# Kernel tuning notes

Measured on AMD Instinct MI355X. Metric: run time of the kernel, lower is better.

The kernel has to match this reference:

```python
import jax, jax.numpy as jnp
import numpy as np

EMBED_DIM = 1024
HEADS = 16
HEAD_DIM = EMBED_DIM // HEADS


def setup_inputs() -> dict:
    key = jax.random.key(0)
    ks = jax.random.split(key, 5)
    B, N, C = 2, 2048, EMBED_DIM
    scale = 1.0 / np.sqrt(C)
    x = jax.random.normal(ks[0], (B, N, C), dtype=jnp.float32)
    W_qkv = jax.random.normal(ks[1], (C, 3 * C), dtype=jnp.float32) * scale
    b_qkv = jax.random.normal(ks[2], (3 * C,), dtype=jnp.float32) * 0.01
    W_out = jax.random.normal(ks[3], (C, C), dtype=jnp.float32) * scale
    b_out = jax.random.normal(ks[4], (C,), dtype=jnp.float32) * 0.01
    return {"x": x, "W_qkv": W_qkv, "b_qkv": b_qkv, "W_out": W_out, "b_out": b_out}


def reference(x, W_qkv, b_qkv, W_out, b_out):
    B, N, C = x.shape
    qkv = x @ W_qkv + b_qkv                      # [B, N, 3C]
    qkv = qkv.reshape(B, N, 3, HEADS, HEAD_DIM)
    qkv = jnp.transpose(qkv, (2, 0, 3, 1, 4))    # [3, B, H, N, d]
    q, k, v = qkv[0], qkv[1], qkv[2]
    attn = jnp.einsum('bhnd,bhmd->bhnm', q, k) / np.sqrt(HEAD_DIM)
    attn = jax.nn.softmax(attn, axis=-1)
    out = jnp.einsum('bhnm,bhmd->bhnd', attn, v)  # [B, H, N, d]
    out = jnp.transpose(out, (0, 2, 1, 3)).reshape(B, N, C)
    return out @ W_out + b_out
```

## Files before the change

### kernel.cpp

```cpp
#include <hip/hip_runtime.h>
#include <stdint.h>

typedef __bf16 bf16_t;
typedef bf16_t bf16x8 __attribute__((ext_vector_type(8)));
typedef bf16_t bf16x2v __attribute__((ext_vector_type(2)));
typedef float f32x4 __attribute__((ext_vector_type(4)));
typedef float f32x16 __attribute__((ext_vector_type(16)));
typedef uint32_t u32x2 __attribute__((ext_vector_type(2)));
typedef uint32_t u32x4 __attribute__((ext_vector_type(4)));

#define BATCH 2
#define SEQ 2048
#define CDIM 1024
#define NH 16
#define HD 64

#define QSCALE 0.18033688011f

__device__ __forceinline__ uint16_t f32_bf16(float f) {
    __bf16 h = (__bf16)f;
    return __builtin_bit_cast(uint16_t, h);
}

__device__ __forceinline__ uint32_t pack_bf16(float a, float b) {
    bf16x2v t;
    t.x = (__bf16)a;
    t.y = (__bf16)b;
    return __builtin_bit_cast(uint32_t, t);
}

__device__ __forceinline__ bf16x8 ld8(const uint16_t* p) {
    return *reinterpret_cast<const bf16x8*>(p);
}

__device__ __forceinline__ void swap32(uint32_t& a, uint32_t& b) {
#if __has_builtin(__builtin_amdgcn_permlane32_swap)
    u32x2 r = __builtin_amdgcn_permlane32_swap(a, b, false, false);
    a = r.x;
    b = r.y;
#else
    asm("v_permlane32_swap_b32 %0, %1" : "+v"(a), "+v"(b));
#endif
}

__device__ __forceinline__ void gld16(const uint16_t* g, uint16_t* l) {
    __builtin_amdgcn_global_load_lds(
        (__attribute__((address_space(1))) void*)(g),
        (__attribute__((address_space(3))) void*)(l), 16, 0, 0);
}

#define LDS_FENCE() asm volatile("s_waitcnt lgkmcnt(0)" ::: "memory")

__global__ __launch_bounds__(256) void prep_kernel(
        const float* __restrict__ x, uint16_t* __restrict__ x_bf,
        const float* __restrict__ Wqkv, uint16_t* __restrict__ wqkvT,
        const float* __restrict__ Wout, uint16_t* __restrict__ woutT) {
    const int bid = blockIdx.x, tid = threadIdx.x;
    if (bid < 4096) {
        int i = (bid * 256 + tid) * 4;
        float4 v = *(const float4*)(x + i);
        ushort4 o;
        o.x = f32_bf16(v.x);
        o.y = f32_bf16(v.y);
        o.z = f32_bf16(v.z);
        o.w = f32_bf16(v.w);
        *(ushort4*)(x_bf + i) = o;
        return;
    }
    __shared__ float tile[32][33];
    const float* in;
    uint16_t* outp;
    int idx, Cc, ncx;
    if (bid < 4096 + 3072) { idx = bid - 4096; in = Wqkv; outp = wqkvT; Cc = 3072; ncx = 96; }
    else                   { idx = bid - 7168; in = Wout; outp = woutT; Cc = 1024; ncx = 32; }
    const int R = 1024;
    int bx = idx % ncx, by = idx / ncx;
    int c0 = bx * 32, r0 = by * 32;
    int tx = tid & 31, ty = tid >> 5;
#pragma unroll
    for (int i = 0; i < 4; i++)
        tile[ty + i * 8][tx] = in[(size_t)(r0 + ty + i * 8) * Cc + c0 + tx];
    __syncthreads();
    const int rr = tid >> 3, seg = tid & 7;
    ushort4 o;
    o.x = f32_bf16(tile[seg * 4 + 0][rr]);
    o.y = f32_bf16(tile[seg * 4 + 1][rr]);
    o.z = f32_bf16(tile[seg * 4 + 2][rr]);
    o.w = f32_bf16(tile[seg * 4 + 3][rr]);
    *(ushort4*)(outp + (size_t)(c0 + rr) * R + r0 + seg * 4) = o;
}

template <int BM, int BN, int MODE>
__global__ __launch_bounds__(256) void gemm_t(
        const uint16_t* __restrict__ A, const uint16_t* __restrict__ Bt, int K,
        const float* __restrict__ bias,
        uint16_t* __restrict__ qw, uint16_t* __restrict__ kw, uint16_t* __restrict__ vt,
        float* __restrict__ out) {
    constexpr int WT_M = BM / 2, WT_N = BN / 2;
    constexpr int MI = WT_M / 16, NJ = WT_N / 16;
    constexpr int ASEG_W = BM / 64, BSEG_W = BN / 64;
    constexpr int AB = 2 * BM * 32 + 2 * BN * 32;
    constexpr int TS = (MODE == 0) ? 4 * 64 * 68 : 0;
    constexpr int SM = AB > TS ? AB : TS;
    __shared__ uint16_t smem[SM];
    uint16_t* As = smem;
    uint16_t* Bs = smem + 2 * BM * 32;

    const int m0 = blockIdx.y * BM, n0 = blockIdx.x * BN;
    const int tid = threadIdx.x;
    const int w = tid >> 6, lane = tid & 63;
    const int quad = lane >> 4, l16 = lane & 15;
    const int wm = (w >> 1) * WT_M, wn = (w & 1) * WT_N;

    const int srow = lane >> 2;
    const int schunk = (lane & 3) ^ (srow & 3);

    const uint16_t* aP[ASEG_W];
    const uint16_t* bP[BSEG_W];
    int aL[ASEG_W], bL[BSEG_W];
#pragma unroll
    for (int s = 0; s < ASEG_W; s++) {
        int seg = w * ASEG_W + s;
        aP[s] = A + (size_t)(m0 + seg * 16 + srow) * K + schunk * 8;
        aL[s] = seg * 512;
    }
#pragma unroll
    for (int s = 0; s < BSEG_W; s++) {
        int seg = w * BSEG_W + s;
        bP[s] = Bt + (size_t)(n0 + seg * 16 + srow) * K + schunk * 8;
        bL[s] = seg * 512;
    }

    auto stage = [&](int buf, int k0) {
#pragma unroll
        for (int s = 0; s < ASEG_W; s++) gld16(aP[s] + k0, As + buf * BM * 32 + aL[s]);
#pragma unroll
        for (int s = 0; s < BSEG_W; s++) gld16(bP[s] + k0, Bs + buf * BN * 32 + bL[s]);
    };

    const int cslot = (quad ^ (l16 & 3)) * 8;
    f32x4 acc[MI][NJ] = {};

    stage(0, 0);
    const int iters = K / 32;
    for (int it = 0; it < iters; ++it) {
        __syncthreads();
        if (it + 1 < iters) stage((it + 1) & 1, (it + 1) * 32);
        const uint16_t* A_ = As + (it & 1) * BM * 32;
        const uint16_t* B_ = Bs + (it & 1) * BN * 32;
        bf16x8 af[MI], bfr[NJ];
#pragma unroll
        for (int i = 0; i < MI; i++) af[i] = ld8(&A_[(wm + i * 16 + l16) * 32 + cslot]);
#pragma unroll
        for (int j = 0; j < NJ; j++) bfr[j] = ld8(&B_[(wn + j * 16 + l16) * 32 + cslot]);
#pragma unroll
        for (int i = 0; i < MI; i++)
#pragma unroll
            for (int j = 0; j < NJ; j++)
                acc[i][j] = __builtin_amdgcn_mfma_f32_16x16x32_bf16(af[i], bfr[j], acc[i][j], 0, 0, 0);
    }

    const int nbase = n0 + wn;
    float bj[NJ];
#pragma unroll
    for (int j = 0; j < NJ; j++) bj[j] = bias[nbase + j * 16 + l16];

    if constexpr (MODE == 1) {
#pragma unroll
        for (int j = 0; j < NJ; j++) {
#pragma unroll
            for (int i = 0; i < MI; i++)
#pragma unroll
                for (int r = 0; r < 4; r++) {
                    int m = m0 + wm + i * 16 + quad * 4 + r;
                    out[(size_t)m * CDIM + nbase + j * 16 + l16] = acc[i][j][r] + bj[j];
                }
        }
    } else {
        __syncthreads();
        uint16_t* T = smem + w * 64 * 68;
        const int gmb = m0 + wm;
        const int b = gmb >> 11, ns0 = gmb & 2047;

        if (nbase < 2048) {
            const int which = nbase >> 10, h = (nbase & 1023) >> 6;
            const float sc = (which == 0) ? QSCALE : 1.0f;
#pragma unroll
            for (int i = 0; i < 4; i++)
#pragma unroll
                for (int j = 0; j < 4; j++)
#pragma unroll
                    for (int r = 0; r < 4; r++)
                        T[(i * 16 + quad * 4 + r) * 68 + j * 16 + l16] =
                            f32_bf16((acc[i][j][r] + bj[j]) * sc);
            LDS_FENCE();
            uint16_t* dst = ((which == 0) ? qw : kw) +
                            (((size_t)b * NH + h) * SEQ + ns0 + lane) * HD;
#pragma unroll
            for (int g = 0; g < 8; g++) {
                bf16x8 v = ld8(&T[lane * 68 + g * 8]);
                *(bf16x8*)(dst + g * 8) = v;
            }
        } else {
#pragma unroll
            for (int i = 0; i < 4; i++)
#pragma unroll
                for (int j = 0; j < 4; j++) {
                    u32x2 pr;
                    pr.x = pack_bf16(acc[i][j][0] + bj[j], acc[i][j][1] + bj[j]);
                    pr.y = pack_bf16(acc[i][j][2] + bj[j], acc[i][j][3] + bj[j]);
                    *(u32x2*)&T[(j * 16 + l16) * 68 + i * 16 + quad * 4] = pr;
                }
            LDS_FENCE();
            const int h = (nbase - 2048) >> 6;
            uint16_t* dst = vt + (((size_t)b * NH + h) * HD + lane) * SEQ + ns0;
#pragma unroll
            for (int g = 0; g < 16; g++) {
                u32x2 d2 = *(const u32x2*)&T[lane * 68 + g * 4];
                *(u32x2*)(dst + g * 4) = d2;
            }
        }
    }
}

__global__ __launch_bounds__(256) void attn_kernel(
        const uint16_t* __restrict__ qg, const uint16_t* __restrict__ kg,
        const uint16_t* __restrict__ vt, uint16_t* __restrict__ og) {
    __shared__ uint16_t Ks[2][128 * 64];
    __shared__ uint16_t Vs[2][64 * 128];

    const int bh = blockIdx.x;
    const int qt = blockIdx.y;
    const int tid = threadIdx.x;
    const int w = tid >> 6, lane = tid & 63;
    const int l32 = lane & 31, hi = lane >> 5;
    const int qrow0 = qt * 128 + w * 32;
    const size_t base = (size_t)bh * SEQ * HD;

    bf16x8 qf[4];
#pragma unroll
    for (int s = 0; s < 4; s++)
        qf[s] = ld8(qg + base + (size_t)(qrow0 + l32) * HD + s * 16 + hi * 8);

    const int krow = lane >> 3;
    const int kch = (lane & 7) ^ krow;
    const int vrow = lane >> 4;
    const uint16_t* ksrc[4];
    const uint16_t* vsrc[4];
#pragma unroll
    for (int s = 0; s < 4; s++) {
        int seg = w * 4 + s;
        ksrc[s] = kg + base + (size_t)(seg * 8 + krow) * HD + kch * 8;
        int vd = seg * 4 + vrow;
        int vch = (lane & 15) ^ (vd & 15);
        vsrc[s] = vt + base + (size_t)vd * SEQ + vch * 8;
    }

    f32x16 o_acc[2] = {};
    f32x16 l_acc = {};
    u32x4 ov;
    ov.x = 0x3F803F80u; ov.y = 0x3F803F80u; ov.z = 0x3F803F80u; ov.w = 0x3F803F80u;
    const bf16x8 ones8 = __builtin_bit_cast(bf16x8, ov);

    auto stage = [&](int buf) {
#pragma unroll
        for (int s = 0; s < 4; s++) {
            int seg = w * 4 + s;
            gld16(ksrc[s], &Ks[buf][seg * 512]);
            ksrc[s] += 128 * HD;
        }
#pragma unroll
        for (int s = 0; s < 4; s++) {
            int seg = w * 4 + s;
            gld16(vsrc[s], &Vs[buf][seg * 512]);
            vsrc[s] += 128;
        }
    };

    stage(0);

    const int kxe = l32 & 7;
    const int vxe = l32 & 15;

    const int NT = SEQ / 128;
    for (int it = 0; it < NT; ++it) {
        __syncthreads();
        if (it + 1 < NT) stage((it + 1) & 1);
        const uint16_t* K_ = Ks[it & 1];
        const uint16_t* V_ = Vs[it & 1];

#pragma unroll
        for (int kvb = 0; kvb < 4; kvb++) {
            f32x16 S = {};
            const uint16_t* Krow = K_ + (kvb * 32 + l32) * 64;
#pragma unroll
            for (int s = 0; s < 4; s++) {
                bf16x8 kf = ld8(Krow + ((2 * s + hi) ^ kxe) * 8);
                S = __builtin_amdgcn_mfma_f32_32x32x16_bf16(kf, qf[s], S, 0, 0, 0);
            }

            uint32_t pk0[4], pk1[4];
#pragma unroll
            for (int c = 0; c < 4; c++) {
                pk0[c] = pack_bf16(__builtin_amdgcn_exp2f(S[4 * c + 0]),
                                   __builtin_amdgcn_exp2f(S[4 * c + 1]));
                pk1[c] = pack_bf16(__builtin_amdgcn_exp2f(S[4 * c + 2]),
                                   __builtin_amdgcn_exp2f(S[4 * c + 3]));
            }

#pragma unroll
            for (int cp = 0; cp < 2; cp++) {
                uint32_t b0 = pk0[2 * cp], b2 = pk0[2 * cp + 1];
                uint32_t b1 = pk1[2 * cp], b3 = pk1[2 * cp + 1];
                swap32(b0, b2);
                swap32(b1, b3);
                u32x4 t;
                t.x = b0; t.y = b1; t.z = b2; t.w = b3;
                bf16x8 pb = __builtin_bit_cast(bf16x8, t);

                l_acc = __builtin_amdgcn_mfma_f32_32x32x16_bf16(ones8, pb, l_acc, 0, 0, 0);
#pragma unroll
                for (int mf = 0; mf < 2; mf++) {
                    int ch = (kvb * 4 + cp * 2 + hi) ^ vxe;
                    bf16x8 vf = ld8(V_ + (mf * 32 + l32) * 128 + ch * 8);
                    o_acc[mf] = __builtin_amdgcn_mfma_f32_32x32x16_bf16(vf, pb, o_acc[mf], 0, 0, 0);
                }
            }
        }
    }

    const int b = bh >> 4, h = bh & 15;
    const float inv = __builtin_amdgcn_rcpf(l_acc[0]);
    const int ns = qrow0 + l32;
    uint16_t* orow = og + (((size_t)b * SEQ + ns) * NH + h) * HD;
#pragma unroll
    for (int mf = 0; mf < 2; mf++)
#pragma unroll
        for (int c = 0; c < 4; c++) {
            u32x2 pr;
            pr.x = pack_bf16(o_acc[mf][4 * c + 0] * inv, o_acc[mf][4 * c + 1] * inv);
            pr.y = pack_bf16(o_acc[mf][4 * c + 2] * inv, o_acc[mf][4 * c + 3] * inv);
            *(u32x2*)(orow + mf * 32 + c * 8 + hi * 4) = pr;
        }
}

extern "C" void kernel_launch(void* const* d_in, const int* in_sizes, int n_in,
                              void* d_out, int out_size, void* d_ws, size_t ws_size,
                              hipStream_t stream) {
    const float* x = (const float*)d_in[0];
    const float* Wqkv = (const float*)d_in[1];
    const float* bqkv = (const float*)d_in[2];
    const float* Wout = (const float*)d_in[3];
    const float* bout = (const float*)d_in[4];
    float* out = (float*)d_out;

    uint16_t* ws = (uint16_t*)d_ws;
    uint16_t* x_bf  = ws;
    uint16_t* wqkvT = x_bf + 4194304;
    uint16_t* woutT = wqkvT + 3145728;
    uint16_t* qw    = woutT + 1048576;
    uint16_t* kw    = qw + 4194304;
    uint16_t* vtw   = kw + 4194304;
    uint16_t* attn  = vtw + 4194304;

    prep_kernel<<<8192, 256, 0, stream>>>(x, x_bf, Wqkv, wqkvT, Wout, woutT);

    gemm_t<128, 128, 0><<<dim3(24, 32), 256, 0, stream>>>(
        x_bf, wqkvT, 1024, bqkv, qw, kw, vtw, nullptr);

    attn_kernel<<<dim3(32, 16), 256, 0, stream>>>(qw, kw, vtw, attn);

    gemm_t<64, 128, 1><<<dim3(8, 64), 256, 0, stream>>>(
        attn, woutT, 1024, bout, nullptr, nullptr, nullptr, out);
}
```

Measured before the change: 185.0 us.

## Software-pipeline QK^T MFMA with softmax and replace ones-MFMA row sum with VALU

```diff
diff --git a/kernel.cpp b/kernel.cpp
--- a/kernel.cpp
+++ b/kernel.cpp
@@ -257,10 +257,7 @@
     }
 
     f32x16 o_acc[2] = {};
-    f32x16 l_acc = {};
-    u32x4 ov;
-    ov.x = 0x3F803F80u; ov.y = 0x3F803F80u; ov.z = 0x3F803F80u; ov.w = 0x3F803F80u;
-    const bf16x8 ones8 = __builtin_bit_cast(bf16x8, ov);
+    float l_red = 0.0f;
 
     auto stage = [&](int buf) {
 #pragma unroll
@@ -281,6 +278,19 @@
 
     const int kxe = l32 & 7;
     const int vxe = l32 & 15;
+    const int krowb = l32 * 64;
+    const int vrowb = l32 * 128;
+    int kco[4];
+#pragma unroll
+    for (int s = 0; s < 4; s++) kco[s] = ((2 * s + hi) ^ kxe) * 8;
+    int vco[4][2];
+#pragma unroll
+    for (int kvb = 0; kvb < 4; kvb++)
+#pragma unroll
+        for (int cp = 0; cp < 2; cp++)
+            vco[kvb][cp] = ((kvb * 4 + cp * 2 + hi) ^ vxe) * 8;
+
+    const f32x16 fzero = {};
 
     const int NT = SEQ / 128;
     for (int it = 0; it < NT; ++it) {
@@ -289,23 +299,53 @@
         const uint16_t* K_ = Ks[it & 1];
         const uint16_t* V_ = Vs[it & 1];
 
+        bf16x8 kf[2][4];
+        f32x16 S[2];
+#pragma unroll
+        for (int s = 0; s < 4; s++) kf[0][s] = ld8(K_ + krowb + kco[s]);
+        S[0] = fzero;
+#pragma unroll
+        for (int s = 0; s < 4; s++)
+            S[0] = __builtin_amdgcn_mfma_f32_32x32x16_bf16(kf[0][s], qf[s], S[0], 0, 0, 0);
+
 #pragma unroll
         for (int kvb = 0; kvb < 4; kvb++) {
-            f32x16 S = {};
-            const uint16_t* Krow = K_ + (kvb * 32 + l32) * 64;
-#pragma unroll
-            for (int s = 0; s < 4; s++) {
-                bf16x8 kf = ld8(Krow + ((2 * s + hi) ^ kxe) * 8);
-                S = __builtin_amdgcn_mfma_f32_32x32x16_bf16(kf, qf[s], S, 0, 0, 0);
-            }
-
+            const int cur = kvb & 1, nxt = cur ^ 1;
+
+            if (kvb < 3) {
+#pragma unroll
+                for (int s = 0; s < 4; s++)
+                    kf[nxt][s] = ld8(K_ + (kvb + 1) * 2048 + krowb + kco[s]);
+            }
+            bf16x8 vf[2][2];
+#pragma unroll
+            for (int cp = 0; cp < 2; cp++)
+#pragma unroll
+                for (int mf = 0; mf < 2; mf++)
+                    vf[cp][mf] = ld8(V_ + vrowb + mf * 4096 + vco[kvb][cp]);
+
+            float p[16];
+#pragma unroll
+            for (int i = 0; i < 16; i++) p[i] = __builtin_amdgcn_exp2f(S[cur][i]);
+            {
+                float s0 = (p[0] + p[1]) + (p[2] + p[3]);
+                float s1 = (p[4] + p[5]) + (p[6] + p[7]);
+                float s2 = (p[8] + p[9]) + (p[10] + p[11]);
+                float s3 = (p[12] + p[13]) + (p[14] + p[15]);
+                l_red += (s0 + s1) + (s2 + s3);
+            }
             uint32_t pk0[4], pk1[4];
 #pragma unroll
             for (int c = 0; c < 4; c++) {
-                pk0[c] = pack_bf16(__builtin_amdgcn_exp2f(S[4 * c + 0]),
-                                   __builtin_amdgcn_exp2f(S[4 * c + 1]));
-                pk1[c] = pack_bf16(__builtin_amdgcn_exp2f(S[4 * c + 2]),
-                                   __builtin_amdgcn_exp2f(S[4 * c + 3]));
+                pk0[c] = pack_bf16(p[4 * c + 0], p[4 * c + 1]);
+                pk1[c] = pack_bf16(p[4 * c + 2], p[4 * c + 3]);
+            }
+
+            if (kvb < 3) {
+                S[nxt] = fzero;
+#pragma unroll
+                for (int s = 0; s < 4; s++)
+                    S[nxt] = __builtin_amdgcn_mfma_f32_32x32x16_bf16(kf[nxt][s], qf[s], S[nxt], 0, 0, 0);
             }
 
 #pragma unroll
@@ -317,20 +357,19 @@
                 u32x4 t;
                 t.x = b0; t.y = b1; t.z = b2; t.w = b3;
                 bf16x8 pb = __builtin_bit_cast(bf16x8, t);
-
-                l_acc = __builtin_amdgcn_mfma_f32_32x32x16_bf16(ones8, pb, l_acc, 0, 0, 0);
-#pragma unroll
-                for (int mf = 0; mf < 2; mf++) {
-                    int ch = (kvb * 4 + cp * 2 + hi) ^ vxe;
-                    bf16x8 vf = ld8(V_ + (mf * 32 + l32) * 128 + ch * 8);
-                    o_acc[mf] = __builtin_amdgcn_mfma_f32_32x32x16_bf16(vf, pb, o_acc[mf], 0, 0, 0);
-                }
-            }
-        }
-    }
+#pragma unroll
+                for (int mf = 0; mf < 2; mf++)
+                    o_acc[mf] = __builtin_amdgcn_mfma_f32_32x32x16_bf16(vf[cp][mf], pb, o_acc[mf], 0, 0, 0);
+            }
+        }
+    }
+
+    uint32_t la = __builtin_bit_cast(uint32_t, l_red), lb = la;
+    swap32(la, lb);
+    const float l_tot = __builtin_bit_cast(float, la) + __builtin_bit_cast(float, lb);
+    const float inv = __builtin_amdgcn_rcpf(l_tot);
 
     const int b = bh >> 4, h = bh & 15;
-    const float inv = __builtin_amdgcn_rcpf(l_acc[0]);
     const int ns = qrow0 + l32;
     uint16_t* orow = og + (((size_t)b * SEQ + ns) * NH + h) * HD;
 #pragma unroll
```

New measurement: 183.6 us. Within noise of the previous version (-0.7%).
